# Optimization experiments

Measured on AMD Instinct MI355X. Metric: run time of the kernel, lower is better.

The kernel has to match this reference:

```python
import jax, jax.numpy as jnp
import numpy as np

B, T, D, U = 32, 1024, 512, 512

def hard_sigmoid(x):
    # Keras hard_sigmoid: clip(0.2*x + 0.5, 0, 1)
    return jnp.clip(x * 0.2 + 0.5, 0.0, 1.0)

def setup_inputs() -> dict:
    key = jax.random.key(0)
    k1, k2, k3 = jax.random.split(key, 3)
    x = jax.random.normal(k1, (B, T, D), dtype=jnp.float32)
    kernel = jax.random.normal(k2, (D, 4 * U), dtype=jnp.float32) * 0.02
    recurrent_kernel = jax.random.normal(k3, (U, 4 * U), dtype=jnp.float32) * 0.02
    # unit_forget_bias: forget-gate slice initialized to 1
    bias = jnp.zeros((4 * U,), dtype=jnp.float32).at[U:2 * U].set(1.0)
    return {"x": x, "kernel": kernel, "recurrent_kernel": recurrent_kernel, "bias": bias}

def reference(x, kernel, recurrent_kernel, bias):
    units = recurrent_kernel.shape[0]
    batch = x.shape[0]
    # Precompute input projections for all timesteps in one big GEMM
    # (implementation=2 style): [B, T, 4U]
    xz = jnp.einsum('btd,dg->btg', x, kernel) + bias
    xz_t = jnp.transpose(xz, (1, 0, 2))  # [T, B, 4U]

    h0 = jnp.zeros((batch, units), dtype=x.dtype)
    c0 = jnp.zeros((batch, units), dtype=x.dtype)

    def step(carry, z_x):
        h, c = carry
        z = z_x + h @ recurrent_kernel  # [B, 4U]
        zi, zf, zc, zo = jnp.split(z, 4, axis=-1)
        i = hard_sigmoid(zi)
        f = hard_sigmoid(zf)
        c_new = f * c + i * jnp.tanh(zc)
        o = hard_sigmoid(zo)
        h_new = o * jnp.tanh(c_new)
        return (h_new, c_new), h_new

    (_, _), hs = jax.lax.scan(step, (h0, c0), xz_t)  # hs: [T, B, U]
    return jnp.transpose(hs, (1, 0, 2))  # [B, T, U] (return_sequences=True)
```

## Files before the change

### kernel.cpp

```cpp
#include <hip/hip_runtime.h>


#define TT 1024
#define DD 512
#define UU 512
#define NCOL 2048
#define SENT 0xFFFFFFFFu
#define RDEPTH 4

__device__ __forceinline__ float hsig(float v) {
  return fminf(fmaxf(0.2f * v + 0.5f, 0.0f), 1.0f);
}
__device__ __forceinline__ float tanh_fast(float x) {
  float e = __expf(2.0f * x);
  return 1.0f - 2.0f / (e + 1.0f);
}

__device__ __forceinline__ void dot64x2_4(
    const float* p0, const float* p1, const float* p2, const float* p3,
    const float (&W)[128],
    float& a00, float& a01, float& a10, float& a11,
    float& a20, float& a21, float& a30, float& a31) {
  a00 = a01 = a10 = a11 = a20 = a21 = a30 = a31 = 0.f;
#pragma unroll
  for (int j4 = 0; j4 < 16; ++j4) {
    float4 v0 = *(const float4*)(p0 + j4 * 4);
    float4 v1 = *(const float4*)(p1 + j4 * 4);
    float4 v2 = *(const float4*)(p2 + j4 * 4);
    float4 v3 = *(const float4*)(p3 + j4 * 4);
    const float* e0 = (const float*)&v0;
    const float* e1 = (const float*)&v1;
    const float* e2 = (const float*)&v2;
    const float* e3 = (const float*)&v3;
#pragma unroll
    for (int jj = 0; jj < 4; ++jj) {
      float w0 = W[2 * (4 * j4 + jj) + 0];
      float w1 = W[2 * (4 * j4 + jj) + 1];
      a00 += e0[jj] * w0; a01 += e0[jj] * w1;
      a10 += e1[jj] * w0; a11 += e1[jj] * w1;
      a20 += e2[jj] * w0; a21 += e2[jj] * w1;
      a30 += e3[jj] * w0; a31 += e3[jj] * w1;
    }
  }
}

template <bool SLEEP>
__device__ __forceinline__ void wavebar(int* ctr, int& ep) {
  asm volatile("s_waitcnt lgkmcnt(0)" ::: "memory");
  if ((threadIdx.x & 63) == 0)
    __hip_atomic_fetch_add(ctr, 1, __ATOMIC_RELAXED, __HIP_MEMORY_SCOPE_WORKGROUP);
  ep += 4;
  while (__hip_atomic_load(ctr, __ATOMIC_RELAXED, __HIP_MEMORY_SCOPE_WORKGROUP) < ep) {
    if (SLEEP) __builtin_amdgcn_s_sleep(1);
  }
  asm volatile("" ::: "memory");
}

__global__ __launch_bounds__(512, 2) void lstm_persistent(
    const float* __restrict__ x,
    const float* __restrict__ Wk,
    const float* __restrict__ Wr,
    const float* __restrict__ bias,
    float* __restrict__ out) {
  const int tid = (int)threadIdx.x;
  const int g   = (int)blockIdx.x & 7;
  const int w   = (int)blockIdx.x >> 3;
  const bool crit = (tid < 256);
  const int idx = tid & 255;
  const int o   = idx >> 5;
  const int col0 = (idx & 31) * 2;
  const int gcol = ((col0 >> 4) * UU) + w * 16 + (col0 & 15);

  const float* M = crit ? Wr : Wk;
  float W[128];
#pragma unroll
  for (int j = 0; j < 64; ++j) {
    float2 ww = *(const float2*)(M + (size_t)(o * 64 + j) * NCOL + gcol);
    W[2 * j] = ww.x; W[2 * j + 1] = ww.y;
  }

  __shared__ float LX[8][4][65];
  __shared__ float LR[2][8][4][65];
  __shared__ float RING[RDEPTH][4][66];
  __shared__ float LH[4][512];
  __shared__ float LB[64];
  __shared__ int cXZdone, cCRITdone, cXZbar, cCRITbar;

  if (tid == 0) { cXZdone = 0; cCRITdone = 0; cXZbar = 0; cCRITbar = 0; }
  if (tid < 64) LB[tid] = bias[(tid >> 4) * UU + w * 16 + (tid & 15)];
  __syncthreads();

  if (crit) {
    const int wv = tid >> 6;
    const int l  = tid & 63;
    const unsigned* ou0 = (const unsigned*)out + (size_t)(g * 4 + 0) * TT * UU;
    const unsigned* ou1 = (const unsigned*)out + (size_t)(g * 4 + 1) * TT * UU;
    const unsigned* ou2 = (const unsigned*)out + (size_t)(g * 4 + 2) * TT * UU;
    const unsigned* ou3 = (const unsigned*)out + (size_t)(g * 4 + 3) * TT * UU;
    const int b_own = tid >> 4;
    const int u_own = tid & 15;
    float c_state = 0.0f;
    int epC = 0;

    for (int t = 0; t < TT; ++t) {
      if (t > 0) {
        const size_t roff = (size_t)(t - 1) * UU + 128 * wv + l;
        unsigned v0, v1, v2, v3, v4, v5, v6, v7;
        for (;;) {
          v0 = __hip_atomic_load(ou0 + roff,      __ATOMIC_RELAXED, __HIP_MEMORY_SCOPE_AGENT);
          v1 = __hip_atomic_load(ou0 + roff + 64, __ATOMIC_RELAXED, __HIP_MEMORY_SCOPE_AGENT);
          v2 = __hip_atomic_load(ou1 + roff,      __ATOMIC_RELAXED, __HIP_MEMORY_SCOPE_AGENT);
          v3 = __hip_atomic_load(ou1 + roff + 64, __ATOMIC_RELAXED, __HIP_MEMORY_SCOPE_AGENT);
          v4 = __hip_atomic_load(ou2 + roff,      __ATOMIC_RELAXED, __HIP_MEMORY_SCOPE_AGENT);
          v5 = __hip_atomic_load(ou2 + roff + 64, __ATOMIC_RELAXED, __HIP_MEMORY_SCOPE_AGENT);
          v6 = __hip_atomic_load(ou3 + roff,      __ATOMIC_RELAXED, __HIP_MEMORY_SCOPE_AGENT);
          v7 = __hip_atomic_load(ou3 + roff + 64, __ATOMIC_RELAXED, __HIP_MEMORY_SCOPE_AGENT);
          int ok = (v0 != SENT) & (v1 != SENT) & (v2 != SENT) & (v3 != SENT) &
                   (v4 != SENT) & (v5 != SENT) & (v6 != SENT) & (v7 != SENT);
          if (__all(ok)) break;
          __builtin_amdgcn_s_sleep(1);
        }
        const int ub = 128 * wv + l;
        LH[0][ub]      = __uint_as_float(v0);
        LH[0][ub + 64] = __uint_as_float(v1);
        LH[1][ub]      = __uint_as_float(v2);
        LH[1][ub + 64] = __uint_as_float(v3);
        LH[2][ub]      = __uint_as_float(v4);
        LH[2][ub + 64] = __uint_as_float(v5);
        LH[3][ub]      = __uint_as_float(v6);
        LH[3][ub + 64] = __uint_as_float(v7);
        asm volatile("s_waitcnt lgkmcnt(0)" ::: "memory");
        __builtin_amdgcn_sched_barrier(0);
        __builtin_amdgcn_s_setprio(1);
        float a00,a01,a10,a11,a20,a21,a30,a31;
        dot64x2_4(&LH[0][o * 64], &LH[1][o * 64], &LH[2][o * 64], &LH[3][o * 64],
                  W, a00,a01,a10,a11,a20,a21,a30,a31);
        const int p = t & 1;
        *(float2*)&LR[p][o][0][col0] = make_float2(a00, a01);
        *(float2*)&LR[p][o][1][col0] = make_float2(a10, a11);
        *(float2*)&LR[p][o][2][col0] = make_float2(a20, a21);
        *(float2*)&LR[p][o][3][col0] = make_float2(a30, a31);
        __builtin_amdgcn_s_setprio(0);
      }
      wavebar<false>(&cCRITbar, epC);
      if (tid < 64) {
        while (__hip_atomic_load(&cXZdone, __ATOMIC_RELAXED,
                                 __HIP_MEMORY_SCOPE_WORKGROUP) < t + 1) {
        }
        asm volatile("" ::: "memory");
        const int s = t & (RDEPTH - 1);
        float s0 = RING[s][b_own][u_own +  0] + LB[u_own +  0];
        float s1 = RING[s][b_own][u_own + 16] + LB[u_own + 16];
        float s2 = RING[s][b_own][u_own + 32] + LB[u_own + 32];
        float s3 = RING[s][b_own][u_own + 48] + LB[u_own + 48];
        if (t > 0) {
          const int p = t & 1;
#pragma unroll
          for (int oo = 0; oo < 8; ++oo) {
            s0 += LR[p][oo][b_own][u_own +  0];
            s1 += LR[p][oo][b_own][u_own + 16];
            s2 += LR[p][oo][b_own][u_own + 32];
            s3 += LR[p][oo][b_own][u_own + 48];
          }
        }
        float gi = hsig(s0);
        float gf = hsig(s1);
        float gc = tanh_fast(s2);
        float go = hsig(s3);
        c_state = gf * c_state + gi * gc;
        float h = go * tanh_fast(c_state);
        __hip_atomic_store(
            out + ((size_t)(g * 4 + b_own) * TT + t) * UU + w * 16 + u_own, h,
            __ATOMIC_RELAXED, __HIP_MEMORY_SCOPE_AGENT);
      }
      if (tid == 0) {
        asm volatile("s_waitcnt lgkmcnt(0)" ::: "memory");
        __hip_atomic_fetch_add(&cCRITdone, 1, __ATOMIC_RELAXED,
                               __HIP_MEMORY_SCOPE_WORKGROUP);
      }
    }
  } else {
    const float* xb0 = x + (size_t)(g * 4 + 0) * TT * DD + o * 64;
    const float* xb1 = x + (size_t)(g * 4 + 1) * TT * DD + o * 64;
    const float* xb2 = x + (size_t)(g * 4 + 2) * TT * DD + o * 64;
    const float* xb3 = x + (size_t)(g * 4 + 3) * TT * DD + o * 64;
    int epX = 0;

    for (int t = 0; t < TT; ++t) {
      size_t off = (size_t)t * DD;
      float a00,a01,a10,a11,a20,a21,a30,a31;
      dot64x2_4(xb0 + off, xb1 + off, xb2 + off, xb3 + off, W,
                a00,a01,a10,a11,a20,a21,a30,a31);
      *(float2*)&LX[o][0][col0] = make_float2(a00, a01);
      *(float2*)&LX[o][1][col0] = make_float2(a10, a11);
      *(float2*)&LX[o][2][col0] = make_float2(a20, a21);
      *(float2*)&LX[o][3][col0] = make_float2(a30, a31);
      wavebar<true>(&cXZbar, epX);
      if (t >= RDEPTH) {
        while (__hip_atomic_load(&cCRITdone, __ATOMIC_RELAXED,
                                 __HIP_MEMORY_SCOPE_WORKGROUP) < t - RDEPTH + 1) {
          __builtin_amdgcn_s_sleep(1);
        }
        asm volatile("" ::: "memory");
      }
      {
        const int b2 = idx >> 6, c3 = idx & 63;
        float ssum = 0.f;
#pragma unroll
        for (int oo = 0; oo < 8; ++oo) ssum += LX[oo][b2][c3];
        RING[t & (RDEPTH - 1)][b2][c3] = ssum;
      }
      wavebar<true>(&cXZbar, epX);
      if (idx == 0) {
        asm volatile("s_waitcnt lgkmcnt(0)" ::: "memory");
        __hip_atomic_fetch_add(&cXZdone, 1, __ATOMIC_RELAXED,
                               __HIP_MEMORY_SCOPE_WORKGROUP);
      }
    }
  }
}

extern "C" void kernel_launch(void* const* d_in, const int* in_sizes, int n_in,
                              void* d_out, int out_size, void* d_ws, size_t ws_size,
                              hipStream_t stream) {
  const float* x    = (const float*)d_in[0];
  const float* Wk   = (const float*)d_in[1];
  const float* Wr   = (const float*)d_in[2];
  const float* bias = (const float*)d_in[3];
  float* out = (float*)d_out;

  hipMemsetAsync(out, 0xFF, (size_t)out_size * sizeof(float), stream);
  lstm_persistent<<<256, 512, 0, stream>>>(x, Wk, Wr, bias, out);
}
```

Before: 4.650 ms.

## Replace sentinel polling of output with per-step canary flags in workspace

Cross-workgroup readiness is now signalled through a small flag array in the workspace (one flag per group, timestep and producer block) instead of polling the output for a sentinel value. This removes the full-output memset and reduces polling traffic to one flag load per lane. The flags are written with relaxed atomics after a vmcnt wait, so ordering of the h stores relative to the flag relies on that wait, which adds a visibility risk. The bias/xz ring reads are also hoisted above the intra-block wave barrier so they overlap the wait. The old sentinel path is kept as a fallback when the workspace is too small.

```diff
diff --git a/kernel.cpp b/kernel.cpp
--- a/kernel.cpp
+++ b/kernel.cpp
@@ -7,6 +7,7 @@
 #define NCOL 2048
 #define SENT 0xFFFFFFFFu
 #define RDEPTH 4
+#define CANARY_WORDS (8 * TT * 32)
 
 __device__ __forceinline__ float hsig(float v) {
   return fminf(fmaxf(0.2f * v + 0.5f, 0.0f), 1.0f);
@@ -61,7 +62,8 @@
     const float* __restrict__ Wk,
     const float* __restrict__ Wr,
     const float* __restrict__ bias,
-    float* __restrict__ out) {
+    float* __restrict__ out,
+    int* __restrict__ canary) {
   const int tid = (int)threadIdx.x;
   const int g   = (int)blockIdx.x & 7;
   const int w   = (int)blockIdx.x >> 3;
@@ -70,6 +72,7 @@
   const int o   = idx >> 5;
   const int col0 = (idx & 31) * 2;
   const int gcol = ((col0 >> 4) * UU) + w * 16 + (col0 & 15);
+  const bool use_canary = (canary != nullptr);
 
   const float* M = crit ? Wr : Wk;
   float W[128];
@@ -106,7 +109,14 @@
       if (t > 0) {
         const size_t roff = (size_t)(t - 1) * UU + 128 * wv + l;
         unsigned v0, v1, v2, v3, v4, v5, v6, v7;
-        for (;;) {
+        if (use_canary) {
+          const int* cp = canary + ((size_t)g * TT + (t - 1)) * 32 + 8 * wv + (l & 7);
+          for (;;) {
+            int fv = __hip_atomic_load(cp, __ATOMIC_RELAXED, __HIP_MEMORY_SCOPE_AGENT);
+            if (__all(fv == 1)) break;
+            __builtin_amdgcn_s_sleep(1);
+          }
+          asm volatile("" ::: "memory");
           v0 = __hip_atomic_load(ou0 + roff,      __ATOMIC_RELAXED, __HIP_MEMORY_SCOPE_AGENT);
           v1 = __hip_atomic_load(ou0 + roff + 64, __ATOMIC_RELAXED, __HIP_MEMORY_SCOPE_AGENT);
           v2 = __hip_atomic_load(ou1 + roff,      __ATOMIC_RELAXED, __HIP_MEMORY_SCOPE_AGENT);
@@ -115,10 +125,21 @@
           v5 = __hip_atomic_load(ou2 + roff + 64, __ATOMIC_RELAXED, __HIP_MEMORY_SCOPE_AGENT);
           v6 = __hip_atomic_load(ou3 + roff,      __ATOMIC_RELAXED, __HIP_MEMORY_SCOPE_AGENT);
           v7 = __hip_atomic_load(ou3 + roff + 64, __ATOMIC_RELAXED, __HIP_MEMORY_SCOPE_AGENT);
-          int ok = (v0 != SENT) & (v1 != SENT) & (v2 != SENT) & (v3 != SENT) &
-                   (v4 != SENT) & (v5 != SENT) & (v6 != SENT) & (v7 != SENT);
-          if (__all(ok)) break;
-          __builtin_amdgcn_s_sleep(1);
+        } else {
+          for (;;) {
+            v0 = __hip_atomic_load(ou0 + roff,      __ATOMIC_RELAXED, __HIP_MEMORY_SCOPE_AGENT);
+            v1 = __hip_atomic_load(ou0 + roff + 64, __ATOMIC_RELAXED, __HIP_MEMORY_SCOPE_AGENT);
+            v2 = __hip_atomic_load(ou1 + roff,      __ATOMIC_RELAXED, __HIP_MEMORY_SCOPE_AGENT);
+            v3 = __hip_atomic_load(ou1 + roff + 64, __ATOMIC_RELAXED, __HIP_MEMORY_SCOPE_AGENT);
+            v4 = __hip_atomic_load(ou2 + roff,      __ATOMIC_RELAXED, __HIP_MEMORY_SCOPE_AGENT);
+            v5 = __hip_atomic_load(ou2 + roff + 64, __ATOMIC_RELAXED, __HIP_MEMORY_SCOPE_AGENT);
+            v6 = __hip_atomic_load(ou3 + roff,      __ATOMIC_RELAXED, __HIP_MEMORY_SCOPE_AGENT);
+            v7 = __hip_atomic_load(ou3 + roff + 64, __ATOMIC_RELAXED, __HIP_MEMORY_SCOPE_AGENT);
+            int ok = (v0 != SENT) & (v1 != SENT) & (v2 != SENT) & (v3 != SENT) &
+                     (v4 != SENT) & (v5 != SENT) & (v6 != SENT) & (v7 != SENT);
+            if (__all(ok)) break;
+            __builtin_amdgcn_s_sleep(1);
+          }
         }
         const int ub = 128 * wv + l;
         LH[0][ub]      = __uint_as_float(v0);
@@ -142,17 +163,20 @@
         *(float2*)&LR[p][o][3][col0] = make_float2(a30, a31);
         __builtin_amdgcn_s_setprio(0);
       }
-      wavebar<false>(&cCRITbar, epC);
+      float s0 = 0.f, s1 = 0.f, s2 = 0.f, s3 = 0.f;
       if (tid < 64) {
         while (__hip_atomic_load(&cXZdone, __ATOMIC_RELAXED,
                                  __HIP_MEMORY_SCOPE_WORKGROUP) < t + 1) {
         }
         asm volatile("" ::: "memory");
         const int s = t & (RDEPTH - 1);
-        float s0 = RING[s][b_own][u_own +  0] + LB[u_own +  0];
-        float s1 = RING[s][b_own][u_own + 16] + LB[u_own + 16];
-        float s2 = RING[s][b_own][u_own + 32] + LB[u_own + 32];
-        float s3 = RING[s][b_own][u_own + 48] + LB[u_own + 48];
+        s0 = RING[s][b_own][u_own +  0] + LB[u_own +  0];
+        s1 = RING[s][b_own][u_own + 16] + LB[u_own + 16];
+        s2 = RING[s][b_own][u_own + 32] + LB[u_own + 32];
+        s3 = RING[s][b_own][u_own + 48] + LB[u_own + 48];
+      }
+      wavebar<false>(&cCRITbar, epC);
+      if (tid < 64) {
         if (t > 0) {
           const int p = t & 1;
 #pragma unroll
@@ -172,6 +196,12 @@
         __hip_atomic_store(
             out + ((size_t)(g * 4 + b_own) * TT + t) * UU + w * 16 + u_own, h,
             __ATOMIC_RELAXED, __HIP_MEMORY_SCOPE_AGENT);
+        if (use_canary) {
+          asm volatile("s_waitcnt vmcnt(0)" ::: "memory");
+          if (tid == 0)
+            __hip_atomic_store(canary + ((size_t)g * TT + t) * 32 + w, 1,
+                               __ATOMIC_RELAXED, __HIP_MEMORY_SCOPE_AGENT);
+        }
       }
       if (tid == 0) {
         asm volatile("s_waitcnt lgkmcnt(0)" ::: "memory");
@@ -229,6 +259,13 @@
   const float* bias = (const float*)d_in[3];
   float* out = (float*)d_out;
 
-  hipMemsetAsync(out, 0xFF, (size_t)out_size * sizeof(float), stream);
-  lstm_persistent<<<256, 512, 0, stream>>>(x, Wk, Wr, bias, out);
-}
+  int* canary = nullptr;
+  const size_t need = (size_t)CANARY_WORDS * sizeof(int);
+  if (ws_size >= need) {
+    canary = (int*)d_ws;
+    hipMemsetAsync(canary, 0, need, stream);
+  } else {
+    hipMemsetAsync(out, 0xFF, (size_t)out_size * sizeof(float), stream);
+  }
+  lstm_persistent<<<256, 512, 0, stream>>>(x, Wk, Wr, bias, out, canary);
+}
```

Measured after the change: 5.365 ms. +15.4%, slower.

## Make each critical wave self-contained for recurrent matvec, removing intra-block barrier

Applied to the files above, without the earlier changes.

Remaps the recurrent-weight ownership so each of the four critical waves computes a complete set of gate columns for its own units. It reduces over K with cross-lane shuffles instead of an LDS partial-sum buffer and a cross-wave barrier. Each wave then applies the gate nonlinearities itself, and the producer waves count per-wave completions. The polling of h from global memory switches to vectorized dwordx4 loads with cache-bypass bits. This shortens the per-timestep critical path but adds shuffle and select overhead and relies on inline asm cache semantics.

```diff
diff --git a/kernel.cpp b/kernel.cpp
--- a/kernel.cpp
+++ b/kernel.cpp
@@ -7,6 +7,8 @@
 #define NCOL 2048
 #define SENT 0xFFFFFFFFu
 #define RDEPTH 4
+
+typedef unsigned int u32x4 __attribute__((ext_vector_type(4)));
 
 __device__ __forceinline__ float hsig(float v) {
   return fminf(fmaxf(0.2f * v + 0.5f, 0.0f), 1.0f);
@@ -66,120 +68,165 @@
   const int g   = (int)blockIdx.x & 7;
   const int w   = (int)blockIdx.x >> 3;
   const bool crit = (tid < 256);
-  const int idx = tid & 255;
-  const int o   = idx >> 5;
-  const int col0 = (idx & 31) * 2;
-  const int gcol = ((col0 >> 4) * UU) + w * 16 + (col0 & 15);
-
-  const float* M = crit ? Wr : Wk;
+  const int l   = tid & 63;
+
+  __shared__ float LX[8][4][65];
+  __shared__ float RING[RDEPTH][4][66];
+  __shared__ float LH[4][8][68];
+  __shared__ float ZB[4][4][18];
+  __shared__ float LB[64];
+  __shared__ int cXZdone, cCRITdone, cXZbar;
+
+  if (tid == 0) { cXZdone = 0; cCRITdone = 0; cXZbar = 0; }
+  if (tid < 64) LB[tid] = bias[(tid >> 4) * UU + w * 16 + (tid & 15)];
+
   float W[128];
-#pragma unroll
-  for (int j = 0; j < 64; ++j) {
-    float2 ww = *(const float2*)(M + (size_t)(o * 64 + j) * NCOL + gcol);
-    W[2 * j] = ww.x; W[2 * j + 1] = ww.y;
-  }
-
-  __shared__ float LX[8][4][65];
-  __shared__ float LR[2][8][4][65];
-  __shared__ float RING[RDEPTH][4][66];
-  __shared__ float LH[4][512];
-  __shared__ float LB[64];
-  __shared__ int cXZdone, cCRITdone, cXZbar, cCRITbar;
-
-  if (tid == 0) { cXZdone = 0; cCRITdone = 0; cXZbar = 0; cCRITbar = 0; }
-  if (tid < 64) LB[tid] = bias[(tid >> 4) * UU + w * 16 + (tid & 15)];
-  __syncthreads();
-
   if (crit) {
     const int wv = tid >> 6;
-    const int l  = tid & 63;
-    const unsigned* ou0 = (const unsigned*)out + (size_t)(g * 4 + 0) * TT * UU;
-    const unsigned* ou1 = (const unsigned*)out + (size_t)(g * 4 + 1) * TT * UU;
-    const unsigned* ou2 = (const unsigned*)out + (size_t)(g * 4 + 2) * TT * UU;
-    const unsigned* ou3 = (const unsigned*)out + (size_t)(g * 4 + 3) * TT * UU;
-    const int b_own = tid >> 4;
-    const int u_own = tid & 15;
+    const int kq = l >> 3;
+    const int cp = l & 7;
+    const int gate = cp >> 1;
+    const int uu2  = (2 * cp) & 3;
+    const int gcb  = gate * UU + w * 16 + 4 * wv + uu2;
+#pragma unroll
+    for (int j = 0; j < 64; ++j) {
+      float2 ww = *(const float2*)(Wr + (size_t)(64 * kq + j) * NCOL + gcb);
+      W[2 * j] = ww.x; W[2 * j + 1] = ww.y;
+    }
+  } else {
+    const int idx = tid & 255;
+    const int o   = idx >> 5;
+    const int col0 = (idx & 31) * 2;
+    const int gcolX = ((col0 >> 4) * UU) + w * 16 + (col0 & 15);
+#pragma unroll
+    for (int j = 0; j < 64; ++j) {
+      float2 ww = *(const float2*)(Wk + (size_t)(o * 64 + j) * NCOL + gcolX);
+      W[2 * j] = ww.x; W[2 * j + 1] = ww.y;
+    }
+  }
+  __syncthreads();
+
+  if (crit) {
+    const int wv  = tid >> 6;
+    const int kq  = l >> 3;
+    const int cp  = l & 7;
+    const int b16 = l >> 4;
+    const int col_l = l & 15;
+    const int gsel = col_l >> 2;
+    const int cc = (col_l >> 2) * 16 + 4 * wv + (col_l & 3);
+    const int b_p  = l >> 4;
+    const int u16p = l & 15;
+    const unsigned* hb = (const unsigned*)out +
+        (size_t)(g * 4 + b_p) * TT * UU + u16p * 4;
     float c_state = 0.0f;
-    int epC = 0;
 
     for (int t = 0; t < TT; ++t) {
+      float zrec = 0.0f;
       if (t > 0) {
-        const size_t roff = (size_t)(t - 1) * UU + 128 * wv + l;
-        unsigned v0, v1, v2, v3, v4, v5, v6, v7;
+        u32x4 d0, d1, d2, d3, d4, d5, d6, d7;
         for (;;) {
-          v0 = __hip_atomic_load(ou0 + roff,      __ATOMIC_RELAXED, __HIP_MEMORY_SCOPE_AGENT);
-          v1 = __hip_atomic_load(ou0 + roff + 64, __ATOMIC_RELAXED, __HIP_MEMORY_SCOPE_AGENT);
-          v2 = __hip_atomic_load(ou1 + roff,      __ATOMIC_RELAXED, __HIP_MEMORY_SCOPE_AGENT);
-          v3 = __hip_atomic_load(ou1 + roff + 64, __ATOMIC_RELAXED, __HIP_MEMORY_SCOPE_AGENT);
-          v4 = __hip_atomic_load(ou2 + roff,      __ATOMIC_RELAXED, __HIP_MEMORY_SCOPE_AGENT);
-          v5 = __hip_atomic_load(ou2 + roff + 64, __ATOMIC_RELAXED, __HIP_MEMORY_SCOPE_AGENT);
-          v6 = __hip_atomic_load(ou3 + roff,      __ATOMIC_RELAXED, __HIP_MEMORY_SCOPE_AGENT);
-          v7 = __hip_atomic_load(ou3 + roff + 64, __ATOMIC_RELAXED, __HIP_MEMORY_SCOPE_AGENT);
-          int ok = (v0 != SENT) & (v1 != SENT) & (v2 != SENT) & (v3 != SENT) &
-                   (v4 != SENT) & (v5 != SENT) & (v6 != SENT) & (v7 != SENT);
+          asm volatile(
+              "global_load_dwordx4 %0, %8, off sc0 sc1\n\t"
+              "global_load_dwordx4 %1, %8, off offset:256 sc0 sc1\n\t"
+              "global_load_dwordx4 %2, %8, off offset:512 sc0 sc1\n\t"
+              "global_load_dwordx4 %3, %8, off offset:768 sc0 sc1\n\t"
+              "global_load_dwordx4 %4, %8, off offset:1024 sc0 sc1\n\t"
+              "global_load_dwordx4 %5, %8, off offset:1280 sc0 sc1\n\t"
+              "global_load_dwordx4 %6, %8, off offset:1536 sc0 sc1\n\t"
+              "global_load_dwordx4 %7, %8, off offset:1792 sc0 sc1\n\t"
+              "s_waitcnt vmcnt(0)"
+              : "=v"(d0), "=v"(d1), "=v"(d2), "=v"(d3),
+                "=v"(d4), "=v"(d5), "=v"(d6), "=v"(d7)
+              : "v"(hb)
+              : "memory");
+          int ok = (d0.x != SENT) & (d0.y != SENT) & (d0.z != SENT) & (d0.w != SENT);
+          ok &= (d1.x != SENT) & (d1.y != SENT) & (d1.z != SENT) & (d1.w != SENT);
+          ok &= (d2.x != SENT) & (d2.y != SENT) & (d2.z != SENT) & (d2.w != SENT);
+          ok &= (d3.x != SENT) & (d3.y != SENT) & (d3.z != SENT) & (d3.w != SENT);
+          ok &= (d4.x != SENT) & (d4.y != SENT) & (d4.z != SENT) & (d4.w != SENT);
+          ok &= (d5.x != SENT) & (d5.y != SENT) & (d5.z != SENT) & (d5.w != SENT);
+          ok &= (d6.x != SENT) & (d6.y != SENT) & (d6.z != SENT) & (d6.w != SENT);
+          ok &= (d7.x != SENT) & (d7.y != SENT) & (d7.z != SENT) & (d7.w != SENT);
           if (__all(ok)) break;
-          __builtin_amdgcn_s_sleep(1);
-        }
-        const int ub = 128 * wv + l;
-        LH[0][ub]      = __uint_as_float(v0);
-        LH[0][ub + 64] = __uint_as_float(v1);
-        LH[1][ub]      = __uint_as_float(v2);
-        LH[1][ub + 64] = __uint_as_float(v3);
-        LH[2][ub]      = __uint_as_float(v4);
-        LH[2][ub + 64] = __uint_as_float(v5);
-        LH[3][ub]      = __uint_as_float(v6);
-        LH[3][ub + 64] = __uint_as_float(v7);
+          __builtin_amdgcn_s_sleep(2);
+        }
+        hb += UU;
+        *(u32x4*)&LH[b_p][0][u16p * 4] = d0;
+        *(u32x4*)&LH[b_p][1][u16p * 4] = d1;
+        *(u32x4*)&LH[b_p][2][u16p * 4] = d2;
+        *(u32x4*)&LH[b_p][3][u16p * 4] = d3;
+        *(u32x4*)&LH[b_p][4][u16p * 4] = d4;
+        *(u32x4*)&LH[b_p][5][u16p * 4] = d5;
+        *(u32x4*)&LH[b_p][6][u16p * 4] = d6;
+        *(u32x4*)&LH[b_p][7][u16p * 4] = d7;
         asm volatile("s_waitcnt lgkmcnt(0)" ::: "memory");
         __builtin_amdgcn_sched_barrier(0);
         __builtin_amdgcn_s_setprio(1);
-        float a00,a01,a10,a11,a20,a21,a30,a31;
-        dot64x2_4(&LH[0][o * 64], &LH[1][o * 64], &LH[2][o * 64], &LH[3][o * 64],
-                  W, a00,a01,a10,a11,a20,a21,a30,a31);
-        const int p = t & 1;
-        *(float2*)&LR[p][o][0][col0] = make_float2(a00, a01);
-        *(float2*)&LR[p][o][1][col0] = make_float2(a10, a11);
-        *(float2*)&LR[p][o][2][col0] = make_float2(a20, a21);
-        *(float2*)&LR[p][o][3][col0] = make_float2(a30, a31);
+        float acc[4][2];
+#pragma unroll
+        for (int b = 0; b < 4; ++b) { acc[b][0] = 0.f; acc[b][1] = 0.f; }
+#pragma unroll
+        for (int b = 0; b < 4; ++b) {
+#pragma unroll
+          for (int j4 = 0; j4 < 16; ++j4) {
+            float4 v = *(const float4*)&LH[b][kq][4 * j4];
+            const float* e = (const float*)&v;
+#pragma unroll
+            for (int jj = 0; jj < 4; ++jj) {
+              acc[b][0] += e[jj] * W[8 * j4 + 2 * jj + 0];
+              acc[b][1] += e[jj] * W[8 * j4 + 2 * jj + 1];
+            }
+          }
+        }
         __builtin_amdgcn_s_setprio(0);
-      }
-      wavebar<false>(&cCRITbar, epC);
-      if (tid < 64) {
-        while (__hip_atomic_load(&cXZdone, __ATOMIC_RELAXED,
-                                 __HIP_MEMORY_SCOPE_WORKGROUP) < t + 1) {
-        }
-        asm volatile("" ::: "memory");
-        const int s = t & (RDEPTH - 1);
-        float s0 = RING[s][b_own][u_own +  0] + LB[u_own +  0];
-        float s1 = RING[s][b_own][u_own + 16] + LB[u_own + 16];
-        float s2 = RING[s][b_own][u_own + 32] + LB[u_own + 32];
-        float s3 = RING[s][b_own][u_own + 48] + LB[u_own + 48];
-        if (t > 0) {
-          const int p = t & 1;
-#pragma unroll
-          for (int oo = 0; oo < 8; ++oo) {
-            s0 += LR[p][oo][b_own][u_own +  0];
-            s1 += LR[p][oo][b_own][u_own + 16];
-            s2 += LR[p][oo][b_own][u_own + 32];
-            s3 += LR[p][oo][b_own][u_own + 48];
-          }
-        }
-        float gi = hsig(s0);
-        float gf = hsig(s1);
-        float gc = tanh_fast(s2);
-        float go = hsig(s3);
-        c_state = gf * c_state + gi * gc;
-        float h = go * tanh_fast(c_state);
-        __hip_atomic_store(
-            out + ((size_t)(g * 4 + b_own) * TT + t) * UU + w * 16 + u_own, h,
-            __ATOMIC_RELAXED, __HIP_MEMORY_SCOPE_AGENT);
-      }
-      if (tid == 0) {
+#pragma unroll
+        for (int b = 0; b < 4; ++b) {
+          acc[b][0] += __shfl_xor(acc[b][0], 8);
+          acc[b][1] += __shfl_xor(acc[b][1], 8);
+          acc[b][0] += __shfl_xor(acc[b][0], 16);
+          acc[b][1] += __shfl_xor(acc[b][1], 16);
+          acc[b][0] += __shfl_xor(acc[b][0], 32);
+          acc[b][1] += __shfl_xor(acc[b][1], 32);
+        }
+        if (l < 8) {
+#pragma unroll
+          for (int b = 0; b < 4; ++b)
+            *(float2*)&ZB[wv][b][2 * l] = make_float2(acc[b][0], acc[b][1]);
+        }
         asm volatile("s_waitcnt lgkmcnt(0)" ::: "memory");
+        zrec = ZB[wv][b16][col_l];
+      }
+      while (__hip_atomic_load(&cXZdone, __ATOMIC_RELAXED,
+                               __HIP_MEMORY_SCOPE_WORKGROUP) < t + 1) {
+      }
+      asm volatile("" ::: "memory");
+      float zfull = zrec + RING[t & (RDEPTH - 1)][b16][cc] + LB[cc];
+      if (l == 0)
         __hip_atomic_fetch_add(&cCRITdone, 1, __ATOMIC_RELAXED,
                                __HIP_MEMORY_SCOPE_WORKGROUP);
+      float za  = __shfl_xor(zfull, 4);
+      float zb  = __shfl_xor(zfull, 8);
+      float zc2 = __shfl_xor(za, 8);
+      float zi  = gsel == 0 ? zfull : gsel == 1 ? za    : gsel == 2 ? zb    : zc2;
+      float zf  = gsel == 0 ? za    : gsel == 1 ? zfull : gsel == 2 ? zc2   : zb;
+      float zc_ = gsel == 0 ? zb    : gsel == 1 ? zc2   : gsel == 2 ? zfull : za;
+      float zo  = gsel == 0 ? zc2   : gsel == 1 ? zb    : gsel == 2 ? za    : zfull;
+      float gi = hsig(zi);
+      float gf = hsig(zf);
+      float gc = tanh_fast(zc_);
+      float go = hsig(zo);
+      c_state = gf * c_state + gi * gc;
+      float h = go * tanh_fast(c_state);
+      if (gsel == 0) {
+        __hip_atomic_store(
+            out + ((size_t)(g * 4 + b16) * TT + t) * UU + w * 16 + 4 * wv + col_l,
+            h, __ATOMIC_RELAXED, __HIP_MEMORY_SCOPE_AGENT);
       }
     }
   } else {
+    const int idx = tid & 255;
+    const int o   = idx >> 5;
+    const int col0 = (idx & 31) * 2;
     const float* xb0 = x + (size_t)(g * 4 + 0) * TT * DD + o * 64;
     const float* xb1 = x + (size_t)(g * 4 + 1) * TT * DD + o * 64;
     const float* xb2 = x + (size_t)(g * 4 + 2) * TT * DD + o * 64;
@@ -188,9 +235,9 @@
 
     for (int t = 0; t < TT; ++t) {
       size_t off = (size_t)t * DD;
-      float a00,a01,a10,a11,a20,a21,a30,a31;
+      float a00, a01, a10, a11, a20, a21, a30, a31;
       dot64x2_4(xb0 + off, xb1 + off, xb2 + off, xb3 + off, W,
-                a00,a01,a10,a11,a20,a21,a30,a31);
+                a00, a01, a10, a11, a20, a21, a30, a31);
       *(float2*)&LX[o][0][col0] = make_float2(a00, a01);
       *(float2*)&LX[o][1][col0] = make_float2(a10, a11);
       *(float2*)&LX[o][2][col0] = make_float2(a20, a21);
@@ -198,7 +245,8 @@
       wavebar<true>(&cXZbar, epX);
       if (t >= RDEPTH) {
         while (__hip_atomic_load(&cCRITdone, __ATOMIC_RELAXED,
-                                 __HIP_MEMORY_SCOPE_WORKGROUP) < t - RDEPTH + 1) {
+                                 __HIP_MEMORY_SCOPE_WORKGROUP) <
+               4 * (t - RDEPTH + 1)) {
           __builtin_amdgcn_s_sleep(1);
         }
         asm volatile("" ::: "memory");
```

Result: slower. 9.752 ms (+109.7%).

## Spread gate epilogue across all critical waves and vectorize dots with packed FMA

Applied to the files above, without the earlier changes.

Reassigns the recurrent-path work so that each of the four critical waves handles one batch row's gate epilogue (16 lanes each) instead of a single wave doing all of it. The RING read and cXZdone wait now happen before the wave barrier. Each wave increments cCRITdone itself, and the producer waits for four times as many counts. The dot products are rewritten with float2 vector types so the compiler can emit packed FMA, and the LH/LR shared layouts are re-indexed with padding. This shortens the serial per-step critical path, at the cost of more atomic traffic on the done counter and a different shared-memory access pattern.

```diff
diff --git a/kernel.cpp b/kernel.cpp
--- a/kernel.cpp
+++ b/kernel.cpp
@@ -8,40 +8,15 @@
 #define SENT 0xFFFFFFFFu
 #define RDEPTH 4
 
+typedef float f32x2 __attribute__((ext_vector_type(2)));
+typedef float f32x4 __attribute__((ext_vector_type(4)));
+
 __device__ __forceinline__ float hsig(float v) {
   return fminf(fmaxf(0.2f * v + 0.5f, 0.0f), 1.0f);
 }
 __device__ __forceinline__ float tanh_fast(float x) {
   float e = __expf(2.0f * x);
   return 1.0f - 2.0f / (e + 1.0f);
-}
-
-__device__ __forceinline__ void dot64x2_4(
-    const float* p0, const float* p1, const float* p2, const float* p3,
-    const float (&W)[128],
-    float& a00, float& a01, float& a10, float& a11,
-    float& a20, float& a21, float& a30, float& a31) {
-  a00 = a01 = a10 = a11 = a20 = a21 = a30 = a31 = 0.f;
-#pragma unroll
-  for (int j4 = 0; j4 < 16; ++j4) {
-    float4 v0 = *(const float4*)(p0 + j4 * 4);
-    float4 v1 = *(const float4*)(p1 + j4 * 4);
-    float4 v2 = *(const float4*)(p2 + j4 * 4);
-    float4 v3 = *(const float4*)(p3 + j4 * 4);
-    const float* e0 = (const float*)&v0;
-    const float* e1 = (const float*)&v1;
-    const float* e2 = (const float*)&v2;
-    const float* e3 = (const float*)&v3;
-#pragma unroll
-    for (int jj = 0; jj < 4; ++jj) {
-      float w0 = W[2 * (4 * j4 + jj) + 0];
-      float w1 = W[2 * (4 * j4 + jj) + 1];
-      a00 += e0[jj] * w0; a01 += e0[jj] * w1;
-      a10 += e1[jj] * w0; a11 += e1[jj] * w1;
-      a20 += e2[jj] * w0; a21 += e2[jj] * w1;
-      a30 += e3[jj] * w0; a31 += e3[jj] * w1;
-    }
-  }
 }
 
 template <bool SLEEP>
@@ -66,39 +41,41 @@
   const int g   = (int)blockIdx.x & 7;
   const int w   = (int)blockIdx.x >> 3;
   const bool crit = (tid < 256);
-  const int idx = tid & 255;
-  const int o   = idx >> 5;
-  const int col0 = (idx & 31) * 2;
-  const int gcol = ((col0 >> 4) * UU) + w * 16 + (col0 & 15);
-
-  const float* M = crit ? Wr : Wk;
-  float W[128];
-#pragma unroll
-  for (int j = 0; j < 64; ++j) {
-    float2 ww = *(const float2*)(M + (size_t)(o * 64 + j) * NCOL + gcol);
-    W[2 * j] = ww.x; W[2 * j + 1] = ww.y;
-  }
+  const int l   = tid & 63;
 
   __shared__ float LX[8][4][65];
-  __shared__ float LR[2][8][4][65];
+  __shared__ float LR[2][8][4][66];
   __shared__ float RING[RDEPTH][4][66];
-  __shared__ float LH[4][512];
+  __shared__ float LH[4][8][68];
   __shared__ float LB[64];
   __shared__ int cXZdone, cCRITdone, cXZbar, cCRITbar;
 
   if (tid == 0) { cXZdone = 0; cCRITdone = 0; cXZbar = 0; cCRITbar = 0; }
   if (tid < 64) LB[tid] = bias[(tid >> 4) * UU + w * 16 + (tid & 15)];
+
+  f32x2 W2[64];
+  {
+    const int wv  = tid >> 6;
+    const int idx = tid & 255;
+    const int cp  = crit ? (l & 31) : (idx & 31);
+    const int ko  = crit ? (2 * (wv & 3) + (l >> 5)) : (idx >> 5);
+    const int gcb = (cp >> 3) * UU + w * 16 + ((2 * cp) & 15);
+    const float* M = crit ? Wr : Wk;
+#pragma unroll
+    for (int j = 0; j < 64; ++j)
+      W2[j] = *(const f32x2*)(M + (size_t)(64 * ko + j) * NCOL + gcb);
+  }
   __syncthreads();
 
   if (crit) {
-    const int wv = tid >> 6;
-    const int l  = tid & 63;
+    const int wv  = tid >> 6;
+    const int kq0 = 2 * wv;
+    const int kql = kq0 + (l >> 5);
+    const int cp  = l & 31;
     const unsigned* ou0 = (const unsigned*)out + (size_t)(g * 4 + 0) * TT * UU;
     const unsigned* ou1 = (const unsigned*)out + (size_t)(g * 4 + 1) * TT * UU;
     const unsigned* ou2 = (const unsigned*)out + (size_t)(g * 4 + 2) * TT * UU;
     const unsigned* ou3 = (const unsigned*)out + (size_t)(g * 4 + 3) * TT * UU;
-    const int b_own = tid >> 4;
-    const int u_own = tid & 15;
     float c_state = 0.0f;
     int epC = 0;
 
@@ -120,47 +97,65 @@
           if (__all(ok)) break;
           __builtin_amdgcn_s_sleep(1);
         }
-        const int ub = 128 * wv + l;
-        LH[0][ub]      = __uint_as_float(v0);
-        LH[0][ub + 64] = __uint_as_float(v1);
-        LH[1][ub]      = __uint_as_float(v2);
-        LH[1][ub + 64] = __uint_as_float(v3);
-        LH[2][ub]      = __uint_as_float(v4);
-        LH[2][ub + 64] = __uint_as_float(v5);
-        LH[3][ub]      = __uint_as_float(v6);
-        LH[3][ub + 64] = __uint_as_float(v7);
+        LH[0][kq0    ][l] = __uint_as_float(v0);
+        LH[0][kq0 + 1][l] = __uint_as_float(v1);
+        LH[1][kq0    ][l] = __uint_as_float(v2);
+        LH[1][kq0 + 1][l] = __uint_as_float(v3);
+        LH[2][kq0    ][l] = __uint_as_float(v4);
+        LH[2][kq0 + 1][l] = __uint_as_float(v5);
+        LH[3][kq0    ][l] = __uint_as_float(v6);
+        LH[3][kq0 + 1][l] = __uint_as_float(v7);
         asm volatile("s_waitcnt lgkmcnt(0)" ::: "memory");
         __builtin_amdgcn_sched_barrier(0);
         __builtin_amdgcn_s_setprio(1);
-        float a00,a01,a10,a11,a20,a21,a30,a31;
-        dot64x2_4(&LH[0][o * 64], &LH[1][o * 64], &LH[2][o * 64], &LH[3][o * 64],
-                  W, a00,a01,a10,a11,a20,a21,a30,a31);
+        f32x2 a0 = {0.f, 0.f}, a1 = {0.f, 0.f}, a2 = {0.f, 0.f}, a3 = {0.f, 0.f};
+#pragma unroll
+        for (int j4 = 0; j4 < 16; ++j4) {
+          f32x4 h0 = *(const f32x4*)&LH[0][kql][4 * j4];
+          f32x4 h1 = *(const f32x4*)&LH[1][kql][4 * j4];
+          f32x4 h2 = *(const f32x4*)&LH[2][kql][4 * j4];
+          f32x4 h3 = *(const f32x4*)&LH[3][kql][4 * j4];
+#pragma unroll
+          for (int jj = 0; jj < 4; ++jj) {
+            f32x2 wj = W2[4 * j4 + jj];
+            a0 += (f32x2){h0[jj], h0[jj]} * wj;
+            a1 += (f32x2){h1[jj], h1[jj]} * wj;
+            a2 += (f32x2){h2[jj], h2[jj]} * wj;
+            a3 += (f32x2){h3[jj], h3[jj]} * wj;
+          }
+        }
+        __builtin_amdgcn_s_setprio(0);
         const int p = t & 1;
-        *(float2*)&LR[p][o][0][col0] = make_float2(a00, a01);
-        *(float2*)&LR[p][o][1][col0] = make_float2(a10, a11);
-        *(float2*)&LR[p][o][2][col0] = make_float2(a20, a21);
-        *(float2*)&LR[p][o][3][col0] = make_float2(a30, a31);
-        __builtin_amdgcn_s_setprio(0);
-      }
-      wavebar<false>(&cCRITbar, epC);
-      if (tid < 64) {
+        *(f32x2*)&LR[p][kql][0][2 * cp] = a0;
+        *(f32x2*)&LR[p][kql][1][2 * cp] = a1;
+        *(f32x2*)&LR[p][kql][2][2 * cp] = a2;
+        *(f32x2*)&LR[p][kql][3][2 * cp] = a3;
+      }
+      float s0 = 0.f, s1 = 0.f, s2 = 0.f, s3 = 0.f;
+      if (l < 16) {
         while (__hip_atomic_load(&cXZdone, __ATOMIC_RELAXED,
                                  __HIP_MEMORY_SCOPE_WORKGROUP) < t + 1) {
         }
         asm volatile("" ::: "memory");
-        const int s = t & (RDEPTH - 1);
-        float s0 = RING[s][b_own][u_own +  0] + LB[u_own +  0];
-        float s1 = RING[s][b_own][u_own + 16] + LB[u_own + 16];
-        float s2 = RING[s][b_own][u_own + 32] + LB[u_own + 32];
-        float s3 = RING[s][b_own][u_own + 48] + LB[u_own + 48];
+        const int ss = t & (RDEPTH - 1);
+        s0 = RING[ss][wv][l +  0] + LB[l +  0];
+        s1 = RING[ss][wv][l + 16] + LB[l + 16];
+        s2 = RING[ss][wv][l + 32] + LB[l + 32];
+        s3 = RING[ss][wv][l + 48] + LB[l + 48];
+      }
+      wavebar<false>(&cCRITbar, epC);
+      if (l == 0)
+        __hip_atomic_fetch_add(&cCRITdone, 1, __ATOMIC_RELAXED,
+                               __HIP_MEMORY_SCOPE_WORKGROUP);
+      if (l < 16) {
         if (t > 0) {
           const int p = t & 1;
 #pragma unroll
-          for (int oo = 0; oo < 8; ++oo) {
-            s0 += LR[p][oo][b_own][u_own +  0];
-            s1 += LR[p][oo][b_own][u_own + 16];
-            s2 += LR[p][oo][b_own][u_own + 32];
-            s3 += LR[p][oo][b_own][u_own + 48];
+          for (int kq = 0; kq < 8; ++kq) {
+            s0 += LR[p][kq][wv][l +  0];
+            s1 += LR[p][kq][wv][l + 16];
+            s2 += LR[p][kq][wv][l + 32];
+            s3 += LR[p][kq][wv][l + 48];
           }
         }
         float gi = hsig(s0);
@@ -170,16 +165,14 @@
         c_state = gf * c_state + gi * gc;
         float h = go * tanh_fast(c_state);
         __hip_atomic_store(
-            out + ((size_t)(g * 4 + b_own) * TT + t) * UU + w * 16 + u_own, h,
+            out + ((size_t)(g * 4 + wv) * TT + t) * UU + w * 16 + l, h,
             __ATOMIC_RELAXED, __HIP_MEMORY_SCOPE_AGENT);
-      }
-      if (tid == 0) {
-        asm volatile("s_waitcnt lgkmcnt(0)" ::: "memory");
-        __hip_atomic_fetch_add(&cCRITdone, 1, __ATOMIC_RELAXED,
-                               __HIP_MEMORY_SCOPE_WORKGROUP);
       }
     }
   } else {
+    const int idx = tid & 255;
+    const int o   = idx >> 5;
+    const int cp  = idx & 31;
     const float* xb0 = x + (size_t)(g * 4 + 0) * TT * DD + o * 64;
     const float* xb1 = x + (size_t)(g * 4 + 1) * TT * DD + o * 64;
     const float* xb2 = x + (size_t)(g * 4 + 2) * TT * DD + o * 64;
@@ -187,18 +180,32 @@
     int epX = 0;
 
     for (int t = 0; t < TT; ++t) {
-      size_t off = (size_t)t * DD;
-      float a00,a01,a10,a11,a20,a21,a30,a31;
-      dot64x2_4(xb0 + off, xb1 + off, xb2 + off, xb3 + off, W,
-                a00,a01,a10,a11,a20,a21,a30,a31);
-      *(float2*)&LX[o][0][col0] = make_float2(a00, a01);
-      *(float2*)&LX[o][1][col0] = make_float2(a10, a11);
-      *(float2*)&LX[o][2][col0] = make_float2(a20, a21);
-      *(float2*)&LX[o][3][col0] = make_float2(a30, a31);
+      const size_t off = (size_t)t * DD;
+      f32x2 a0 = {0.f, 0.f}, a1 = {0.f, 0.f}, a2 = {0.f, 0.f}, a3 = {0.f, 0.f};
+#pragma unroll
+      for (int j4 = 0; j4 < 16; ++j4) {
+        f32x4 v0 = *(const f32x4*)(xb0 + off + 4 * j4);
+        f32x4 v1 = *(const f32x4*)(xb1 + off + 4 * j4);
+        f32x4 v2 = *(const f32x4*)(xb2 + off + 4 * j4);
+        f32x4 v3 = *(const f32x4*)(xb3 + off + 4 * j4);
+#pragma unroll
+        for (int jj = 0; jj < 4; ++jj) {
+          f32x2 wj = W2[4 * j4 + jj];
+          a0 += (f32x2){v0[jj], v0[jj]} * wj;
+          a1 += (f32x2){v1[jj], v1[jj]} * wj;
+          a2 += (f32x2){v2[jj], v2[jj]} * wj;
+          a3 += (f32x2){v3[jj], v3[jj]} * wj;
+        }
+      }
+      *(f32x2*)&LX[o][0][2 * cp] = a0;
+      *(f32x2*)&LX[o][1][2 * cp] = a1;
+      *(f32x2*)&LX[o][2][2 * cp] = a2;
+      *(f32x2*)&LX[o][3][2 * cp] = a3;
       wavebar<true>(&cXZbar, epX);
       if (t >= RDEPTH) {
         while (__hip_atomic_load(&cCRITdone, __ATOMIC_RELAXED,
-                                 __HIP_MEMORY_SCOPE_WORKGROUP) < t - RDEPTH + 1) {
+                                 __HIP_MEMORY_SCOPE_WORKGROUP) <
+               4 * (t - RDEPTH + 1)) {
           __builtin_amdgcn_s_sleep(1);
         }
         asm volatile("" ::: "memory");
```

Measured after the change: 4.274 ms. 1.09x faster.
